# Performance work log

Hardware: AMD Instinct MI355X
Metric: run time of the kernel (lower is better)

Reference implementation:

```python
import jax, jax.numpy as jnp
import numpy as np

BN_EPS = 1e-5

def batchnorm(x, gamma, beta):
    # training-mode BatchNorm1d over the row (node/sample) dimension
    mu = jnp.mean(x, axis=0)
    var = jnp.var(x, axis=0)
    return (x - mu) * jax.lax.rsqrt(var + BN_EPS) * gamma + beta

def gin_mean(h, src, dst, n):
    # DGL GINConv(apply_func=None, aggregator='mean', eps=0):
    # h_new = h + mean_{u in N(v)} h_u
    ones = jnp.ones((src.shape[0],), h.dtype)
    deg = jax.ops.segment_sum(ones, dst, num_segments=n)
    agg = jax.ops.segment_sum(h[src], dst, num_segments=n)
    return h + agg / jnp.maximum(deg, 1.0)[:, None]

def setup_inputs() -> dict:
    key = jax.random.key(0)
    ks = jax.random.split(key, 12)
    N, E, B, K = 10000, 160000, 64, 10
    DIN, D, DH = 20, 512, 256
    x = jax.random.normal(ks[0], (N, DIN), dtype=jnp.float32)
    edge_src = jax.random.randint(ks[1], (E,), 0, N, dtype=jnp.int32)
    edge_dst = jax.random.randint(ks[2], (E,), 0, N, dtype=jnp.int32)
    node2graph = jnp.sort(jax.random.randint(ks[3], (N,), 0, B, dtype=jnp.int32))
    pg_emb = jax.random.normal(ks[4], (B, D), dtype=jnp.float32)
    neigh_emb = jax.random.normal(ks[5], (B, K, D), dtype=jnp.float32)
    s = lambda i, shp: jax.random.normal(ks[i], shp, dtype=jnp.float32) * 0.02
    return dict(
        x=x, pg_emb=pg_emb, neigh_emb=neigh_emb,
        W_init=s(6, (DIN, D)), b_init=jnp.zeros((D,), jnp.float32),
        g1=jnp.ones((D,), jnp.float32), be1=jnp.zeros((D,), jnp.float32),
        g2=jnp.ones((D,), jnp.float32), be2=jnp.zeros((D,), jnp.float32),
        W_fc=s(7, (3 * D, DH)), b_fc=jnp.zeros((DH,), jnp.float32),
        W_fc2=s(8, (DH, DH)), b_fc2=jnp.zeros((DH,), jnp.float32),
        W_fc3=s(9, (DH, DH)), b_fc3=jnp.zeros((DH,), jnp.float32),
        W_fc4=s(10, (DH, 1)), b_fc4=jnp.zeros((1,), jnp.float32),
        gb=jnp.ones((DH,), jnp.float32), bb=jnp.zeros((DH,), jnp.float32),
        gb2=jnp.ones((DH,), jnp.float32), bb2=jnp.zeros((DH,), jnp.float32),
        gb3=jnp.ones((DH,), jnp.float32), bb3=jnp.zeros((DH,), jnp.float32),
        edge_src=edge_src, edge_dst=edge_dst, node2graph=node2graph,
    )

def reference(x, pg_emb, neigh_emb, W_init, b_init, g1, be1, g2, be2,
              W_fc, b_fc, W_fc2, b_fc2, W_fc3, b_fc3, W_fc4, b_fc4,
              gb, bb, gb2, bb2, gb3, bb3, edge_src, edge_dst, node2graph):
    N = x.shape[0]
    B, K, D = neigh_emb.shape
    # two GIN(mean) layers with BN+ReLU on the batched graph
    h = x @ W_init + b_init                                   # [N, 512]
    h = jax.nn.relu(batchnorm(gin_mean(h, edge_src, edge_dst, N), g1, be1))
    h = jax.nn.relu(batchnorm(gin_mean(h, edge_src, edge_dst, N), g2, be2))
    # dgl.mean_nodes: per-graph mean readout
    cnt = jax.ops.segment_sum(jnp.ones((N,), h.dtype), node2graph, num_segments=B)
    qemb = jax.ops.segment_sum(h, node2graph, num_segments=B) / jnp.maximum(cnt, 1.0)[:, None]
    a = jnp.concatenate([qemb, pg_emb], axis=1)               # [B, 2D]
    a = jnp.broadcast_to(a[:, None, :], (B, K, 2 * D))        # repeat per candidate
    b = jnp.concatenate([a, neigh_emb], axis=-1).reshape(B * K, 3 * D)
    H = jax.nn.relu(batchnorm(b @ W_fc + b_fc, gb, bb))
    H2 = jax.nn.relu(batchnorm(H @ W_fc2 + b_fc2, gb2, bb2))
    H3 = jax.nn.relu(batchnorm(H2 @ W_fc3 + b_fc3, gb3, bb3))
    pred = jax.nn.sigmoid(H3 @ W_fc4 + b_fc4)                 # [B*K, 1]
    return pred.reshape(B, K)
```

## Files before the change

kernel.cpp:

```cpp
#include <hip/hip_runtime.h>
#include <hip/hip_bf16.h>
#include <math.h>

#define N_NODES 10000
#define N_EDGES 160000
#define D 512
#define DIN 20
#define B 64
#define KC 10
#define DH 256
#define NROW (B*KC)
#define BN_EPS 1e-5f

#define ZCOUNT 36352
#define Z4 (ZCOUNT/4)
#define D4 (N_NODES/4)
#define IM_ROWS 8
#define IM_UNITS (N_NODES/IM_ROWS)
#define GWAVES 4
#define GBLOCKS 1250
#define F1_NS 6
#define F1_ROWS 8
#define F1_KS 256

struct P {
  const float *x, *pg, *neigh, *Winit, *binit;
  const float *g1, *be1, *g2, *be2;
  const float *Wfc, *bfc, *W2, *b2, *W3, *b3, *W4, *b4;
  const float *gbA, *bbA, *gbB, *bbB, *gbC, *bbC;
  const int *esrc, *edst, *n2g;
  unsigned short *hb0, *hb1, *hb2;
  float *zbuf, *csum1, *csq1, *csum2, *csq2;
  float *s1,*q1,*s2,*q2,*s3,*q3, *qemb;
  float *G1,*G2,*G3,*part;
  int *degi,*rowstart,*cursor,*csr,*gstart;
  float *out;
};

__device__ __forceinline__ void f4acc(float4& a, const float4 v){
  a.x += v.x; a.y += v.y; a.z += v.z; a.w += v.w;
}
__device__ __forceinline__ void mk_affine(const float4 s, const float4 q, const float4 g,
                                          const float4 b, float4& sc, float4& sh){
  const float invN = 1.0f/(float)N_NODES;
  float mu, var, rs;
  mu = s.x*invN; var = q.x*invN - mu*mu; rs = rsqrtf(var+BN_EPS); sc.x = rs*g.x; sh.x = b.x - mu*sc.x;
  mu = s.y*invN; var = q.y*invN - mu*mu; rs = rsqrtf(var+BN_EPS); sc.y = rs*g.y; sh.y = b.y - mu*sc.y;
  mu = s.z*invN; var = q.z*invN - mu*mu; rs = rsqrtf(var+BN_EPS); sc.z = rs*g.z; sh.z = b.z - mu*sc.z;
  mu = s.w*invN; var = q.w*invN - mu*mu; rs = rsqrtf(var+BN_EPS); sc.w = rs*g.w; sh.w = b.w - mu*sc.w;
}
__device__ __forceinline__ float4 aff_relu(const float4 v, const float4 sc, const float4 sh){
  float4 o;
  o.x = fmaxf(fmaf(v.x, sc.x, sh.x), 0.0f);
  o.y = fmaxf(fmaf(v.y, sc.y, sh.y), 0.0f);
  o.z = fmaxf(fmaf(v.z, sc.z, sh.z), 0.0f);
  o.w = fmaxf(fmaf(v.w, sc.w, sh.w), 0.0f);
  return o;
}
__device__ __forceinline__ void bf_unpack(const uint4 u, float4& lo, float4& hi){
  lo.x = __uint_as_float(u.x << 16); lo.y = __uint_as_float(u.x & 0xffff0000u);
  lo.z = __uint_as_float(u.y << 16); lo.w = __uint_as_float(u.y & 0xffff0000u);
  hi.x = __uint_as_float(u.z << 16); hi.y = __uint_as_float(u.z & 0xffff0000u);
  hi.z = __uint_as_float(u.w << 16); hi.w = __uint_as_float(u.w & 0xffff0000u);
}
__device__ __forceinline__ unsigned bf_pack2(float a, float b){
  unsigned ua = __float_as_uint(a); ua = (ua + 0x7fffu + ((ua>>16)&1u)) >> 16;
  unsigned ub = __float_as_uint(b); ub = (ub + 0x7fffu + ((ub>>16)&1u)) & 0xffff0000u;
  return (ua & 0xffffu) | ub;
}
__device__ __forceinline__ unsigned short bf_pack1(float a){
  unsigned ua = __float_as_uint(a); return (unsigned short)((ua + 0x7fffu + ((ua>>16)&1u)) >> 16);
}

__global__ __launch_bounds__(256) void k_setup(P p){
  int b = blockIdx.x, nb = gridDim.x, t = threadIdx.x;
  for (int i4 = b*256 + t; i4 < Z4 + D4; i4 += nb*256){
    if (i4 < Z4) ((float4*)p.zbuf)[i4] = make_float4(0.f,0.f,0.f,0.f);
    else         ((int4*)p.degi)[i4 - Z4] = make_int4(0,0,0,0);
  }
  if (b == 0 && t <= B){
    int lo = 0, hi = N_NODES;
    while (lo < hi){ int mid = (lo+hi)>>1; if (p.n2g[mid] < t) lo = mid+1; else hi = mid; }
    p.gstart[t] = lo;
  }
}

__global__ __launch_bounds__(256) void k_deg(P p){
  int e = blockIdx.x*256 + threadIdx.x;
  if (e < N_EDGES) atomicAdd(&p.degi[p.edst[e]], 1);
}

__global__ __launch_bounds__(256) void k_scan(P p){
  __shared__ int part[256];
  int t = threadIdx.x;
  const int PER = (N_NODES + 255)/256;
  int base = t*PER;
  int s = 0;
  for (int i = 0; i < PER; ++i){ int idx = base+i; if (idx < N_NODES) s += p.degi[idx]; }
  part[t] = s;
  __syncthreads();
  for (int off = 1; off < 256; off <<= 1){
    int v = (t >= off) ? part[t-off] : 0;
    __syncthreads();
    part[t] += v;
    __syncthreads();
  }
  int run = (t > 0) ? part[t-1] : 0;
  for (int i = 0; i < PER; ++i){
    int idx = base+i;
    if (idx < N_NODES){ p.rowstart[idx] = run; p.cursor[idx] = run; run += p.degi[idx]; }
  }
  if (t == 255) p.rowstart[N_NODES] = run;
}

__global__ __launch_bounds__(256) void k_fill(P p){
  int e = blockIdx.x*256 + threadIdx.x;
  if (e < N_EDGES){
    int pos = atomicAdd(&p.cursor[p.edst[e]], 1);
    p.csr[pos] = p.esrc[e];
  }
}

__global__ __launch_bounds__(256) void k_init(P p){
  __shared__ float xs[IM_ROWS*DIN];
  int t = threadIdx.x;
  float wlo[DIN], whi[DIN];
  #pragma unroll
  for (int k = 0; k < DIN; ++k){ wlo[k] = p.Winit[k*D + t]; whi[k] = p.Winit[k*D + t + 256]; }
  float b0 = p.binit[t], b1 = p.binit[t+256];
  int r0 = blockIdx.x*IM_ROWS;
  for (int i = t; i < IM_ROWS*DIN; i += 256) xs[i] = p.x[(size_t)r0*DIN + i];
  __syncthreads();
  for (int rr = 0; rr < IM_ROWS; ++rr){
    float a0 = b0, a1 = b1;
    #pragma unroll
    for (int k = 0; k < DIN; ++k){
      float xv = xs[rr*DIN + k];
      a0 += xv*wlo[k]; a1 += xv*whi[k];
    }
    p.hb0[(size_t)(r0+rr)*D + t]       = bf_pack1(a0);
    p.hb0[(size_t)(r0+rr)*D + t + 256] = bf_pack1(a1);
  }
}

template<bool FUSED>
__device__ __forceinline__ void gather_body(const P& p,
    const unsigned short* __restrict__ hin, unsigned short* __restrict__ hout,
    const float* pcs, const float* pcq, const float* pgm, const float* pbt,
    float* cs, float* cq, float* red){
  int t = threadIdx.x;
  int lane = t & 63;
  int wave = t >> 6;
  int wid  = blockIdx.x*GWAVES + wave;
  int tot  = gridDim.x*GWAVES;
  const uint4* hb4 = (const uint4*)hin;
  float4 scA, shA, scB, shB;
  if (FUSED){
    mk_affine(((const float4*)pcs)[2*lane],   ((const float4*)pcq)[2*lane],
              ((const float4*)pgm)[2*lane],   ((const float4*)pbt)[2*lane],   scA, shA);
    mk_affine(((const float4*)pcs)[2*lane+1], ((const float4*)pcq)[2*lane+1],
              ((const float4*)pgm)[2*lane+1], ((const float4*)pbt)[2*lane+1], scB, shB);
  }
  float4 sLo = make_float4(0,0,0,0), sHi = make_float4(0,0,0,0);
  float4 qLo = make_float4(0,0,0,0), qHi = make_float4(0,0,0,0);
  for (int node = wid; node < N_NODES; node += tot){
    int start = p.rowstart[node], end = p.rowstart[node+1];
    float4 aLo = make_float4(0,0,0,0), aHi = make_float4(0,0,0,0);
    float4 bLo = make_float4(0,0,0,0), bHi = make_float4(0,0,0,0);
    for (int base = start; base < end; base += 64){
      int cnt = end - base; if (cnt > 64) cnt = 64;
      int myidx = (lane < cnt) ? p.csr[base+lane] : 0;
      int j = 0;
      for (; j+8 <= cnt; j += 8){
        uint4 u[8];
        #pragma unroll
        for (int k = 0; k < 8; ++k){
          int idx = __shfl(myidx, j+k, 64);
          u[k] = hb4[(size_t)idx*64 + lane];
        }
        #pragma unroll
        for (int k = 0; k < 8; ++k){
          float4 lo, hi; bf_unpack(u[k], lo, hi);
          if (FUSED){ lo = aff_relu(lo, scA, shA); hi = aff_relu(hi, scB, shB); }
          if (k & 1){ f4acc(bLo, lo); f4acc(bHi, hi); }
          else      { f4acc(aLo, lo); f4acc(aHi, hi); }
        }
      }
      for (; j < cnt; ++j){
        int idx = __shfl(myidx, j, 64);
        uint4 u0 = hb4[(size_t)idx*64 + lane];
        float4 lo, hi; bf_unpack(u0, lo, hi);
        if (FUSED){ lo = aff_relu(lo, scA, shA); hi = aff_relu(hi, scB, shB); }
        f4acc(aLo, lo); f4acc(aHi, hi);
      }
    }
    float inv = 1.0f/fmaxf((float)(end-start), 1.0f);
    uint4 us = hb4[(size_t)node*64 + lane];
    float4 hLo, hHi; bf_unpack(us, hLo, hHi);
    if (FUSED){ hLo = aff_relu(hLo, scA, shA); hHi = aff_relu(hHi, scB, shB); }
    float4 oLo, oHi;
    oLo.x = hLo.x + (aLo.x+bLo.x)*inv;  oLo.y = hLo.y + (aLo.y+bLo.y)*inv;
    oLo.z = hLo.z + (aLo.z+bLo.z)*inv;  oLo.w = hLo.w + (aLo.w+bLo.w)*inv;
    oHi.x = hHi.x + (aHi.x+bHi.x)*inv;  oHi.y = hHi.y + (aHi.y+bHi.y)*inv;
    oHi.z = hHi.z + (aHi.z+bHi.z)*inv;  oHi.w = hHi.w + (aHi.w+bHi.w)*inv;
    uint4 ou;
    ou.x = bf_pack2(oLo.x, oLo.y); ou.y = bf_pack2(oLo.z, oLo.w);
    ou.z = bf_pack2(oHi.x, oHi.y); ou.w = bf_pack2(oHi.z, oHi.w);
    ((uint4*)hout)[(size_t)node*64 + lane] = ou;
    f4acc(sLo, oLo); f4acc(sHi, oHi);
    qLo.x += oLo.x*oLo.x; qLo.y += oLo.y*oLo.y; qLo.z += oLo.z*oLo.z; qLo.w += oLo.w*oLo.w;
    qHi.x += oHi.x*oHi.x; qHi.y += oHi.y*oHi.y; qHi.z += oHi.z*oHi.z; qHi.w += oHi.w*oHi.w;
  }
  float* my = red + wave*1024;
  int c = 8*lane;
  *((float4*)&my[c])      = sLo;  *((float4*)&my[c+4])     = sHi;
  *((float4*)&my[512+c])  = qLo;  *((float4*)&my[512+c+4]) = qHi;
  __syncthreads();
  for (int e = t; e < 1024; e += 256){
    float v = red[e] + red[1024+e] + red[2048+e] + red[3072+e];
    if (e < 512) atomicAdd(&cs[e], v);
    else         atomicAdd(&cq[e-512], v);
  }
}

__global__ __launch_bounds__(256) void k_g1(P p){
  __shared__ float red[4096];
  gather_body<false>(p, p.hb0, p.hb1, nullptr,nullptr,nullptr,nullptr, p.csum1, p.csq1, red);
}
__global__ __launch_bounds__(256) void k_g2(P p){
  __shared__ float red[4096];
  gather_body<true>(p, p.hb1, p.hb2, p.csum1, p.csq1, p.g1, p.be1, p.csum2, p.csq2, red);
}

__global__ __launch_bounds__(256) void k_readout(P p){
  __shared__ float red[2048];
  int g = blockIdx.x >> 3, chunk = blockIdx.x & 7;
  int t = threadIdx.x;
  int lane = t & 63, wave = t >> 6;
  const uint4* hb4 = (const uint4*)p.hb2;
  float4 scA, shA, scB, shB;
  mk_affine(((const float4*)p.csum2)[2*lane],   ((const float4*)p.csq2)[2*lane],
            ((const float4*)p.g2)[2*lane],      ((const float4*)p.be2)[2*lane],   scA, shA);
  mk_affine(((const float4*)p.csum2)[2*lane+1], ((const float4*)p.csq2)[2*lane+1],
            ((const float4*)p.g2)[2*lane+1],    ((const float4*)p.be2)[2*lane+1], scB, shB);
  int s = p.gstart[g], e = p.gstart[g+1];
  int rows = e - s;
  int per = (rows + 7)/8;
  int r0 = s + chunk*per;
  int r1 = r0 + per; if (r1 > e) r1 = e;
  float4 aLo = make_float4(0,0,0,0), aHi = make_float4(0,0,0,0);
  for (int r = r0 + wave; r < r1; r += 4){
    uint4 u = hb4[(size_t)r*64 + lane];
    float4 lo, hi; bf_unpack(u, lo, hi);
    lo = aff_relu(lo, scA, shA); hi = aff_relu(hi, scB, shB);
    f4acc(aLo, lo); f4acc(aHi, hi);
  }
  int c = 8*lane;
  *((float4*)&red[wave*512 + c])     = aLo;
  *((float4*)&red[wave*512 + c + 4]) = aHi;
  __syncthreads();
  for (int e2 = t; e2 < 512; e2 += 256){
    float v = red[e2] + red[512+e2] + red[1024+e2] + red[1536+e2];
    atomicAdd(&p.qemb[(size_t)g*D + e2], v);
  }
}

__global__ __launch_bounds__(256) void k_fc1(P p){
  __shared__ float brow[F1_ROWS*F1_KS];
  int t = threadIdx.x;
  int rb = blockIdx.x % 80, ks = blockIdx.x / 80;
  int r0 = rb*F1_ROWS, k0 = ks*F1_KS;
  for (int rr = 0; rr < F1_ROWS; ++rr){
    int r = r0+rr;
    int g = r/KC, k = r - g*KC;
    int j = k0 + t;
    float v;
    if (j < D){
      float invc = 1.0f/fmaxf((float)(p.gstart[g+1]-p.gstart[g]), 1.0f);
      v = p.qemb[(size_t)g*D + j]*invc;
    } else if (j < 2*D){
      v = p.pg[(size_t)g*D + (j-D)];
    } else {
      v = p.neigh[((size_t)g*KC + k)*D + (j-2*D)];
    }
    brow[rr*F1_KS + t] = v;
  }
  __syncthreads();
  float acc[F1_ROWS] = {0.f,0.f,0.f,0.f,0.f,0.f,0.f,0.f};
  #pragma unroll 4
  for (int kk = 0; kk < F1_KS; ++kk){
    float w = p.Wfc[(size_t)(k0+kk)*DH + t];
    #pragma unroll
    for (int rr = 0; rr < F1_ROWS; ++rr) acc[rr] += brow[rr*F1_KS + kk]*w;
  }
  for (int rr = 0; rr < F1_ROWS; ++rr)
    p.part[((size_t)ks*NROW + r0+rr)*DH + t] = acc[rr];
}

__global__ __launch_bounds__(256) void k_reduce(P p){
  int t = threadIdx.x;
  int r0 = blockIdx.x*8;
  float bval = p.bfc[t];
  float ls = 0.f, lq = 0.f;
  for (int rr = 0; rr < 8; ++rr){
    int r = r0+rr;
    float acc = bval;
    for (int sl = 0; sl < F1_NS; ++sl) acc += p.part[((size_t)sl*NROW + r)*DH + t];
    p.G1[(size_t)r*DH + t] = acc;
    ls += acc; lq += acc*acc;
  }
  atomicAdd(&p.s1[t], ls); atomicAdd(&p.q1[t], lq);
}

__device__ __forceinline__ void fcmid_body(const float* in, const float* ps, const float* pq,
    const float* gamma, const float* beta, const float* W, const float* bias,
    float* outG, float* s, float* q, float* row){
  int t = threadIdx.x;
  int r = blockIdx.x;
  const float invM = 1.0f/(float)NROW;
  {
    float mu = ps[t]*invM;
    float var = pq[t]*invM - mu*mu;
    float rs = rsqrtf(var + BN_EPS);
    float v = in[(size_t)r*DH + t];
    row[t] = fmaxf((v-mu)*rs*gamma[t] + beta[t], 0.0f);
  }
  __syncthreads();
  float acc = bias[t];
  #pragma unroll 8
  for (int kk = 0; kk < DH; ++kk)
    acc += row[kk]*W[(size_t)kk*DH + t];
  outG[(size_t)r*DH + t] = acc;
  atomicAdd(&s[t], acc); atomicAdd(&q[t], acc*acc);
}
__global__ __launch_bounds__(256) void k_fc2(P p){ __shared__ float row[DH];
  fcmid_body(p.G1, p.s1, p.q1, p.gbA, p.bbA, p.W2, p.b2, p.G2, p.s2, p.q2, row); }
__global__ __launch_bounds__(256) void k_fc3(P p){ __shared__ float row[DH];
  fcmid_body(p.G2, p.s2, p.q2, p.gbB, p.bbB, p.W3, p.b3, p.G3, p.s3, p.q3, row); }

__global__ __launch_bounds__(256) void k_final(P p){
  int t = threadIdx.x;
  int wave = t>>6, lane = t&63;
  int r = blockIdx.x*4 + wave;
  const float invM = 1.0f/(float)NROW;
  float sum = 0.f;
  #pragma unroll
  for (int j = 0; j < 4; ++j){
    int c = lane + 64*j;
    float mu = p.s3[c]*invM;
    float var = p.q3[c]*invM - mu*mu;
    float rs = rsqrtf(var+BN_EPS);
    float v = p.G3[(size_t)r*DH + c];
    v = fmaxf((v-mu)*rs*p.gbC[c] + p.bbC[c], 0.0f);
    sum += v*p.W4[c];
  }
  #pragma unroll
  for (int off = 32; off > 0; off >>= 1) sum += __shfl_down(sum, off, 64);
  if (lane == 0){
    float z = sum + p.b4[0];
    p.out[r] = 1.0f/(1.0f + expf(-z));
  }
}

extern "C" void kernel_launch(void* const* d_in, const int* in_sizes, int n_in,
                              void* d_out, int out_size, void* d_ws, size_t ws_size,
                              hipStream_t stream) {
  P p;
  p.x     = (const float*)d_in[0];
  p.pg    = (const float*)d_in[1];
  p.neigh = (const float*)d_in[2];
  p.Winit = (const float*)d_in[3];
  p.binit = (const float*)d_in[4];
  p.g1    = (const float*)d_in[5];
  p.be1   = (const float*)d_in[6];
  p.g2    = (const float*)d_in[7];
  p.be2   = (const float*)d_in[8];
  p.Wfc   = (const float*)d_in[9];
  p.bfc   = (const float*)d_in[10];
  p.W2    = (const float*)d_in[11];
  p.b2    = (const float*)d_in[12];
  p.W3    = (const float*)d_in[13];
  p.b3    = (const float*)d_in[14];
  p.W4    = (const float*)d_in[15];
  p.b4    = (const float*)d_in[16];
  p.gbA   = (const float*)d_in[17];
  p.bbA   = (const float*)d_in[18];
  p.gbB   = (const float*)d_in[19];
  p.bbB   = (const float*)d_in[20];
  p.gbC   = (const float*)d_in[21];
  p.bbC   = (const float*)d_in[22];
  p.esrc  = (const int*)d_in[23];
  p.edst  = (const int*)d_in[24];
  p.n2g   = (const int*)d_in[25];
  p.out   = (float*)d_out;

  float* ws = (float*)d_ws;
  size_t off = 0;
  p.hb0 = (unsigned short*)(ws + off); off += (size_t)N_NODES*D/2;
  p.hb1 = (unsigned short*)(ws + off); off += (size_t)N_NODES*D/2;
  p.hb2 = (unsigned short*)(ws + off); off += (size_t)N_NODES*D/2;
  p.zbuf  = ws + off;
  p.csum1 = ws + off; off += 512;
  p.csq1  = ws + off; off += 512;
  p.csum2 = ws + off; off += 512;
  p.csq2  = ws + off; off += 512;
  p.s1    = ws + off; off += 256;
  p.q1    = ws + off; off += 256;
  p.s2    = ws + off; off += 256;
  p.q2    = ws + off; off += 256;
  p.s3    = ws + off; off += 256;
  p.q3    = ws + off; off += 256;
  p.qemb  = ws + off; off += (size_t)B*D;
  p.G1   = ws + off; off += (size_t)NROW*DH;
  p.G2   = ws + off; off += (size_t)NROW*DH;
  p.G3   = ws + off; off += (size_t)NROW*DH;
  p.part = ws + off; off += (size_t)F1_NS*NROW*DH;
  p.degi     = (int*)(ws + off); off += N_NODES;
  p.rowstart = (int*)(ws + off); off += N_NODES + 1;
  p.cursor   = (int*)(ws + off); off += N_NODES;
  p.csr      = (int*)(ws + off); off += N_EDGES;
  p.gstart   = (int*)(ws + off); off += B + 1;

  k_setup<<<64, 256, 0, stream>>>(p);
  k_deg<<<(N_EDGES+255)/256, 256, 0, stream>>>(p);
  k_scan<<<1, 256, 0, stream>>>(p);
  k_init<<<IM_UNITS, 256, 0, stream>>>(p);
  k_fill<<<(N_EDGES+255)/256, 256, 0, stream>>>(p);
  k_g1<<<GBLOCKS, 256, 0, stream>>>(p);
  k_g2<<<GBLOCKS, 256, 0, stream>>>(p);
  k_readout<<<512, 256, 0, stream>>>(p);
  k_fc1<<<480, 256, 0, stream>>>(p);
  k_reduce<<<80, 256, 0, stream>>>(p);
  k_fc2<<<NROW, 256, 0, stream>>>(p);
  k_fc3<<<NROW, 256, 0, stream>>>(p);
  k_final<<<NROW/4, 256, 0, stream>>>(p);
}
```

Before: 255.3 us.

## Software-pipeline neighbor gathers over two nodes per wave and fuse degree with init

The gather kernel now gives each wave exactly two nodes and interleaves their neighbor loads using double-buffered batches of eight rows. Predicated weights replace the tail loops, which raises memory-level parallelism in the latency-bound gather. The degree-count kernel is also merged into the initial projection kernel as extra blocks, removing one launch. The gather hardcodes 2 nodes per wave times 5000 waves, so it depends on GBLOCKS exactly covering N_NODES, and the deeper buffering raises register pressure.

```diff
diff --git a/kernel.cpp b/kernel.cpp
--- a/kernel.cpp
+++ b/kernel.cpp
@@ -17,6 +17,7 @@
 #define D4 (N_NODES/4)
 #define IM_ROWS 8
 #define IM_UNITS (N_NODES/IM_ROWS)
+#define DEG_BLOCKS 625
 #define GWAVES 4
 #define GBLOCKS 1250
 #define F1_NS 6
@@ -72,6 +73,140 @@
   unsigned ua = __float_as_uint(a); return (unsigned short)((ua + 0x7fffu + ((ua>>16)&1u)) >> 16);
 }
 
+struct Batch { uint4 v[8]; };
+
+__device__ __forceinline__ void load8(Batch& b, const uint4* __restrict__ hb4,
+                                      int idxreg, int k, int c, int lane){
+  #pragma unroll
+  for (int j = 0; j < 8; ++j){
+    int r = k*8 + j;
+    int ri = (r < c) ? r : (c-1);
+    int idx = __builtin_amdgcn_readlane(idxreg, ri);
+    b.v[j] = hb4[(size_t)idx*64 + lane];
+  }
+}
+
+template<bool FUSED>
+__device__ __forceinline__ void cons8(const Batch& b, int k, int c,
+    float4& accLo, float4& accHi,
+    const float4& scA, const float4& shA, const float4& scB, const float4& shB){
+  #pragma unroll
+  for (int j = 0; j < 8; ++j){
+    int r = k*8 + j;
+    float w = (r < c) ? 1.0f : 0.0f;
+    float4 lo, hi; bf_unpack(b.v[j], lo, hi);
+    if (FUSED){ lo = aff_relu(lo, scA, shA); hi = aff_relu(hi, scB, shB); }
+    accLo.x = fmaf(lo.x, w, accLo.x); accLo.y = fmaf(lo.y, w, accLo.y);
+    accLo.z = fmaf(lo.z, w, accLo.z); accLo.w = fmaf(lo.w, w, accLo.w);
+    accHi.x = fmaf(hi.x, w, accHi.x); accHi.y = fmaf(hi.y, w, accHi.y);
+    accHi.z = fmaf(hi.z, w, accHi.z); accHi.w = fmaf(hi.w, w, accHi.w);
+  }
+}
+
+template<bool FUSED>
+__device__ __forceinline__ void gather_body(const P& p,
+    const unsigned short* __restrict__ hin, unsigned short* __restrict__ hout,
+    const float* pcs, const float* pcq, const float* pgm, const float* pbt,
+    float* cs, float* cq, float* red){
+  int t = threadIdx.x;
+  int lane = t & 63;
+  int wave = t >> 6;
+  int wid  = blockIdx.x*GWAVES + wave;
+  int nA = 2*wid, nB = nA + 1;
+  const uint4* hb4 = (const uint4*)hin;
+  uint4 uSA = hb4[(size_t)nA*64 + lane];
+  uint4 uSB = hb4[(size_t)nB*64 + lane];
+  float4 scA, shA, scB, shB;
+  if (FUSED){
+    mk_affine(((const float4*)pcs)[2*lane],   ((const float4*)pcq)[2*lane],
+              ((const float4*)pgm)[2*lane],   ((const float4*)pbt)[2*lane],   scA, shA);
+    mk_affine(((const float4*)pcs)[2*lane+1], ((const float4*)pcq)[2*lane+1],
+              ((const float4*)pgm)[2*lane+1], ((const float4*)pbt)[2*lane+1], scB, shB);
+  }
+  int sA = p.rowstart[nA], sB = p.rowstart[nB], eB = p.rowstart[nB+1];
+  int cA = sB - sA, cB = eB - sB;
+  int idxA = (lane < cA) ? p.csr[sA + lane] : 0;
+  int idxB = (lane < cB) ? p.csr[sB + lane] : 0;
+  int cAf = (cA > 64) ? 64 : cA;
+  int cBf = (cB > 64) ? 64 : cB;
+  int bA = (cAf + 7) >> 3, bB = (cBf + 7) >> 3;
+  Batch A0, A1, B0, B1;
+  if (bA > 0) load8(A0, hb4, idxA, 0, cAf, lane);
+  if (bB > 0) load8(B0, hb4, idxB, 0, cBf, lane);
+  if (bA > 1) load8(A1, hb4, idxA, 1, cAf, lane);
+  if (bB > 1) load8(B1, hb4, idxB, 1, cBf, lane);
+  float4 aLoA = make_float4(0,0,0,0), aHiA = make_float4(0,0,0,0);
+  float4 aLoB = make_float4(0,0,0,0), aHiB = make_float4(0,0,0,0);
+  int ta = 0, tb = 0;
+  while (ta < bA || tb < bB){
+    if (ta < bA){ cons8<FUSED>(A0, ta, cAf, aLoA, aHiA, scA, shA, scB, shB);
+                  if (ta+2 < bA) load8(A0, hb4, idxA, ta+2, cAf, lane); ta++; }
+    if (tb < bB){ cons8<FUSED>(B0, tb, cBf, aLoB, aHiB, scA, shA, scB, shB);
+                  if (tb+2 < bB) load8(B0, hb4, idxB, tb+2, cBf, lane); tb++; }
+    if (ta < bA){ cons8<FUSED>(A1, ta, cAf, aLoA, aHiA, scA, shA, scB, shB);
+                  if (ta+2 < bA) load8(A1, hb4, idxA, ta+2, cAf, lane); ta++; }
+    if (tb < bB){ cons8<FUSED>(B1, tb, cBf, aLoB, aHiB, scA, shA, scB, shB);
+                  if (tb+2 < bB) load8(B1, hb4, idxB, tb+2, cBf, lane); tb++; }
+  }
+  for (int base = 64; base < cA; base += 64){
+    int cnt = cA - base; if (cnt > 64) cnt = 64;
+    int mi = (lane < cnt) ? p.csr[sA + base + lane] : 0;
+    for (int j = 0; j < cnt; ++j){
+      int idx = __builtin_amdgcn_readlane(mi, j);
+      uint4 u = hb4[(size_t)idx*64 + lane];
+      float4 lo, hi; bf_unpack(u, lo, hi);
+      if (FUSED){ lo = aff_relu(lo, scA, shA); hi = aff_relu(hi, scB, shB); }
+      f4acc(aLoA, lo); f4acc(aHiA, hi);
+    }
+  }
+  for (int base = 64; base < cB; base += 64){
+    int cnt = cB - base; if (cnt > 64) cnt = 64;
+    int mi = (lane < cnt) ? p.csr[sB + base + lane] : 0;
+    for (int j = 0; j < cnt; ++j){
+      int idx = __builtin_amdgcn_readlane(mi, j);
+      uint4 u = hb4[(size_t)idx*64 + lane];
+      float4 lo, hi; bf_unpack(u, lo, hi);
+      if (FUSED){ lo = aff_relu(lo, scA, shA); hi = aff_relu(hi, scB, shB); }
+      f4acc(aLoB, lo); f4acc(aHiB, hi);
+    }
+  }
+  float4 sLo = make_float4(0,0,0,0), sHi = make_float4(0,0,0,0);
+  float4 qLo = make_float4(0,0,0,0), qHi = make_float4(0,0,0,0);
+  #pragma unroll
+  for (int n = 0; n < 2; ++n){
+    int node = (n == 0) ? nA : nB;
+    int cnt  = (n == 0) ? cA : cB;
+    uint4 us = (n == 0) ? uSA : uSB;
+    float4 sumLo = (n == 0) ? aLoA : aLoB;
+    float4 sumHi = (n == 0) ? aHiA : aHiB;
+    float inv = 1.0f/fmaxf((float)cnt, 1.0f);
+    float4 hLo, hHi; bf_unpack(us, hLo, hHi);
+    if (FUSED){ hLo = aff_relu(hLo, scA, shA); hHi = aff_relu(hHi, scB, shB); }
+    float4 oLo, oHi;
+    oLo.x = hLo.x + sumLo.x*inv;  oLo.y = hLo.y + sumLo.y*inv;
+    oLo.z = hLo.z + sumLo.z*inv;  oLo.w = hLo.w + sumLo.w*inv;
+    oHi.x = hHi.x + sumHi.x*inv;  oHi.y = hHi.y + sumHi.y*inv;
+    oHi.z = hHi.z + sumHi.z*inv;  oHi.w = hHi.w + sumHi.w*inv;
+    uint4 ou;
+    ou.x = bf_pack2(oLo.x, oLo.y); ou.y = bf_pack2(oLo.z, oLo.w);
+    ou.z = bf_pack2(oHi.x, oHi.y); ou.w = bf_pack2(oHi.z, oHi.w);
+    ((uint4*)hout)[(size_t)node*64 + lane] = ou;
+    f4acc(sLo, oLo); f4acc(sHi, oHi);
+    qLo.x += oLo.x*oLo.x; qLo.y += oLo.y*oLo.y; qLo.z += oLo.z*oLo.z; qLo.w += oLo.w*oLo.w;
+    qHi.x += oHi.x*oHi.x; qHi.y += oHi.y*oHi.y; qHi.z += oHi.z*oHi.z; qHi.w += oHi.w*oHi.w;
+  }
+  float* my = red + wave*1024;
+  int c = 8*lane;
+  *((float4*)&my[c])      = sLo;  *((float4*)&my[c+4])     = sHi;
+  *((float4*)&my[512+c])  = qLo;  *((float4*)&my[512+c+4]) = qHi;
+  __syncthreads();
+  for (int e = t; e < 1024; e += 256){
+    float v = red[e] + red[1024+e] + red[2048+e] + red[3072+e];
+    if (e < 512) atomicAdd(&cs[e], v);
+    else         atomicAdd(&cq[e-512], v);
+  }
+}
+
 __global__ __launch_bounds__(256) void k_setup(P p){
   int b = blockIdx.x, nb = gridDim.x, t = threadIdx.x;
   for (int i4 = b*256 + t; i4 < Z4 + D4; i4 += nb*256){
@@ -85,50 +220,20 @@
   }
 }
 
-__global__ __launch_bounds__(256) void k_deg(P p){
-  int e = blockIdx.x*256 + threadIdx.x;
-  if (e < N_EDGES) atomicAdd(&p.degi[p.edst[e]], 1);
-}
-
-__global__ __launch_bounds__(256) void k_scan(P p){
-  __shared__ int part[256];
-  int t = threadIdx.x;
-  const int PER = (N_NODES + 255)/256;
-  int base = t*PER;
-  int s = 0;
-  for (int i = 0; i < PER; ++i){ int idx = base+i; if (idx < N_NODES) s += p.degi[idx]; }
-  part[t] = s;
-  __syncthreads();
-  for (int off = 1; off < 256; off <<= 1){
-    int v = (t >= off) ? part[t-off] : 0;
-    __syncthreads();
-    part[t] += v;
-    __syncthreads();
-  }
-  int run = (t > 0) ? part[t-1] : 0;
-  for (int i = 0; i < PER; ++i){
-    int idx = base+i;
-    if (idx < N_NODES){ p.rowstart[idx] = run; p.cursor[idx] = run; run += p.degi[idx]; }
-  }
-  if (t == 255) p.rowstart[N_NODES] = run;
-}
-
-__global__ __launch_bounds__(256) void k_fill(P p){
-  int e = blockIdx.x*256 + threadIdx.x;
-  if (e < N_EDGES){
-    int pos = atomicAdd(&p.cursor[p.edst[e]], 1);
-    p.csr[pos] = p.esrc[e];
-  }
-}
-
-__global__ __launch_bounds__(256) void k_init(P p){
+__global__ __launch_bounds__(256) void k_deg_init(P p){
   __shared__ float xs[IM_ROWS*DIN];
   int t = threadIdx.x;
+  if (blockIdx.x < DEG_BLOCKS){
+    int e = blockIdx.x*256 + t;
+    if (e < N_EDGES) atomicAdd(&p.degi[p.edst[e]], 1);
+    return;
+  }
+  int unit = blockIdx.x - DEG_BLOCKS;
   float wlo[DIN], whi[DIN];
   #pragma unroll
   for (int k = 0; k < DIN; ++k){ wlo[k] = p.Winit[k*D + t]; whi[k] = p.Winit[k*D + t + 256]; }
   float b0 = p.binit[t], b1 = p.binit[t+256];
-  int r0 = blockIdx.x*IM_ROWS;
+  int r0 = unit*IM_ROWS;
   for (int i = t; i < IM_ROWS*DIN; i += 256) xs[i] = p.x[(size_t)r0*DIN + i];
   __syncthreads();
   for (int rr = 0; rr < IM_ROWS; ++rr){
@@ -143,83 +248,34 @@
   }
 }
 
-template<bool FUSED>
-__device__ __forceinline__ void gather_body(const P& p,
-    const unsigned short* __restrict__ hin, unsigned short* __restrict__ hout,
-    const float* pcs, const float* pcq, const float* pgm, const float* pbt,
-    float* cs, float* cq, float* red){
-  int t = threadIdx.x;
-  int lane = t & 63;
-  int wave = t >> 6;
-  int wid  = blockIdx.x*GWAVES + wave;
-  int tot  = gridDim.x*GWAVES;
-  const uint4* hb4 = (const uint4*)hin;
-  float4 scA, shA, scB, shB;
-  if (FUSED){
-    mk_affine(((const float4*)pcs)[2*lane],   ((const float4*)pcq)[2*lane],
-              ((const float4*)pgm)[2*lane],   ((const float4*)pbt)[2*lane],   scA, shA);
-    mk_affine(((const float4*)pcs)[2*lane+1], ((const float4*)pcq)[2*lane+1],
-              ((const float4*)pgm)[2*lane+1], ((const float4*)pbt)[2*lane+1], scB, shB);
-  }
-  float4 sLo = make_float4(0,0,0,0), sHi = make_float4(0,0,0,0);
-  float4 qLo = make_float4(0,0,0,0), qHi = make_float4(0,0,0,0);
-  for (int node = wid; node < N_NODES; node += tot){
-    int start = p.rowstart[node], end = p.rowstart[node+1];
-    float4 aLo = make_float4(0,0,0,0), aHi = make_float4(0,0,0,0);
-    float4 bLo = make_float4(0,0,0,0), bHi = make_float4(0,0,0,0);
-    for (int base = start; base < end; base += 64){
-      int cnt = end - base; if (cnt > 64) cnt = 64;
-      int myidx = (lane < cnt) ? p.csr[base+lane] : 0;
-      int j = 0;
-      for (; j+8 <= cnt; j += 8){
-        uint4 u[8];
-        #pragma unroll
-        for (int k = 0; k < 8; ++k){
-          int idx = __shfl(myidx, j+k, 64);
-          u[k] = hb4[(size_t)idx*64 + lane];
-        }
-        #pragma unroll
-        for (int k = 0; k < 8; ++k){
-          float4 lo, hi; bf_unpack(u[k], lo, hi);
-          if (FUSED){ lo = aff_relu(lo, scA, shA); hi = aff_relu(hi, scB, shB); }
-          if (k & 1){ f4acc(bLo, lo); f4acc(bHi, hi); }
-          else      { f4acc(aLo, lo); f4acc(aHi, hi); }
-        }
-      }
-      for (; j < cnt; ++j){
-        int idx = __shfl(myidx, j, 64);
-        uint4 u0 = hb4[(size_t)idx*64 + lane];
-        float4 lo, hi; bf_unpack(u0, lo, hi);
-        if (FUSED){ lo = aff_relu(lo, scA, shA); hi = aff_relu(hi, scB, shB); }
-        f4acc(aLo, lo); f4acc(aHi, hi);
-      }
-    }
-    float inv = 1.0f/fmaxf((float)(end-start), 1.0f);
-    uint4 us = hb4[(size_t)node*64 + lane];
-    float4 hLo, hHi; bf_unpack(us, hLo, hHi);
-    if (FUSED){ hLo = aff_relu(hLo, scA, shA); hHi = aff_relu(hHi, scB, shB); }
-    float4 oLo, oHi;
-    oLo.x = hLo.x + (aLo.x+bLo.x)*inv;  oLo.y = hLo.y + (aLo.y+bLo.y)*inv;
-    oLo.z = hLo.z + (aLo.z+bLo.z)*inv;  oLo.w = hLo.w + (aLo.w+bLo.w)*inv;
-    oHi.x = hHi.x + (aHi.x+bHi.x)*inv;  oHi.y = hHi.y + (aHi.y+bHi.y)*inv;
-    oHi.z = hHi.z + (aHi.z+bHi.z)*inv;  oHi.w = hHi.w + (aHi.w+bHi.w)*inv;
-    uint4 ou;
-    ou.x = bf_pack2(oLo.x, oLo.y); ou.y = bf_pack2(oLo.z, oLo.w);
-    ou.z = bf_pack2(oHi.x, oHi.y); ou.w = bf_pack2(oHi.z, oHi.w);
-    ((uint4*)hout)[(size_t)node*64 + lane] = ou;
-    f4acc(sLo, oLo); f4acc(sHi, oHi);
-    qLo.x += oLo.x*oLo.x; qLo.y += oLo.y*oLo.y; qLo.z += oLo.z*oLo.z; qLo.w += oLo.w*oLo.w;
-    qHi.x += oHi.x*oHi.x; qHi.y += oHi.y*oHi.y; qHi.z += oHi.z*oHi.z; qHi.w += oHi.w*oHi.w;
-  }
-  float* my = red + wave*1024;
-  int c = 8*lane;
-  *((float4*)&my[c])      = sLo;  *((float4*)&my[c+4])     = sHi;
-  *((float4*)&my[512+c])  = qLo;  *((float4*)&my[512+c+4]) = qHi;
-  __syncthreads();
-  for (int e = t; e < 1024; e += 256){
-    float v = red[e] + red[1024+e] + red[2048+e] + red[3072+e];
-    if (e < 512) atomicAdd(&cs[e], v);
-    else         atomicAdd(&cq[e-512], v);
+__global__ __launch_bounds__(256) void k_scan(P p){
+  __shared__ int part[256];
+  int t = threadIdx.x;
+  const int PER = (N_NODES + 255)/256;
+  int base = t*PER;
+  int s = 0;
+  for (int i = 0; i < PER; ++i){ int idx = base+i; if (idx < N_NODES) s += p.degi[idx]; }
+  part[t] = s;
+  __syncthreads();
+  for (int off = 1; off < 256; off <<= 1){
+    int v = (t >= off) ? part[t-off] : 0;
+    __syncthreads();
+    part[t] += v;
+    __syncthreads();
+  }
+  int run = (t > 0) ? part[t-1] : 0;
+  for (int i = 0; i < PER; ++i){
+    int idx = base+i;
+    if (idx < N_NODES){ p.rowstart[idx] = run; p.cursor[idx] = run; run += p.degi[idx]; }
+  }
+  if (t == 255) p.rowstart[N_NODES] = run;
+}
+
+__global__ __launch_bounds__(256) void k_fill(P p){
+  int e = blockIdx.x*256 + threadIdx.x;
+  if (e < N_EDGES){
+    int pos = atomicAdd(&p.cursor[p.edst[e]], 1);
+    p.csr[pos] = p.esrc[e];
   }
 }
 
@@ -422,9 +478,8 @@
   p.gstart   = (int*)(ws + off); off += B + 1;
 
   k_setup<<<64, 256, 0, stream>>>(p);
-  k_deg<<<(N_EDGES+255)/256, 256, 0, stream>>>(p);
+  k_deg_init<<<DEG_BLOCKS + IM_UNITS, 256, 0, stream>>>(p);
   k_scan<<<1, 256, 0, stream>>>(p);
-  k_init<<<IM_UNITS, 256, 0, stream>>>(p);
   k_fill<<<(N_EDGES+255)/256, 256, 0, stream>>>(p);
   k_g1<<<GBLOCKS, 256, 0, stream>>>(p);
   k_g2<<<GBLOCKS, 256, 0, stream>>>(p);
```

After: 252.9 us. No clear change (-0.9%).

## Merge degree count with init matmul and split-K tile FC2/FC3 with row reuse

Applied to the files above, without the earlier changes.

The degree-count and input-projection kernels become one launch, with block ranges assigned to each task. This removes a launch and lets the two run at the same time. FC2 and FC3 now compute 4 rows per block over a 2-way K split, so each loaded weight is reused across rows. The partial results go to a buffer and a shared reduce kernel adds the bias and accumulates the BN statistics. This cuts weight traffic and per-row atomics but adds two extra reduce launches.

```diff
diff --git a/kernel.cpp b/kernel.cpp
--- a/kernel.cpp
+++ b/kernel.cpp
@@ -17,11 +17,15 @@
 #define D4 (N_NODES/4)
 #define IM_ROWS 8
 #define IM_UNITS (N_NODES/IM_ROWS)
+#define DEG_BLOCKS 625
 #define GWAVES 4
 #define GBLOCKS 1250
 #define F1_NS 6
 #define F1_ROWS 8
 #define F1_KS 256
+#define FM_ROWS 4
+#define FM_KS 128
+#define FM_NS 2
 
 struct P {
   const float *x, *pg, *neigh, *Winit, *binit;
@@ -70,77 +74,6 @@
 }
 __device__ __forceinline__ unsigned short bf_pack1(float a){
   unsigned ua = __float_as_uint(a); return (unsigned short)((ua + 0x7fffu + ((ua>>16)&1u)) >> 16);
-}
-
-__global__ __launch_bounds__(256) void k_setup(P p){
-  int b = blockIdx.x, nb = gridDim.x, t = threadIdx.x;
-  for (int i4 = b*256 + t; i4 < Z4 + D4; i4 += nb*256){
-    if (i4 < Z4) ((float4*)p.zbuf)[i4] = make_float4(0.f,0.f,0.f,0.f);
-    else         ((int4*)p.degi)[i4 - Z4] = make_int4(0,0,0,0);
-  }
-  if (b == 0 && t <= B){
-    int lo = 0, hi = N_NODES;
-    while (lo < hi){ int mid = (lo+hi)>>1; if (p.n2g[mid] < t) lo = mid+1; else hi = mid; }
-    p.gstart[t] = lo;
-  }
-}
-
-__global__ __launch_bounds__(256) void k_deg(P p){
-  int e = blockIdx.x*256 + threadIdx.x;
-  if (e < N_EDGES) atomicAdd(&p.degi[p.edst[e]], 1);
-}
-
-__global__ __launch_bounds__(256) void k_scan(P p){
-  __shared__ int part[256];
-  int t = threadIdx.x;
-  const int PER = (N_NODES + 255)/256;
-  int base = t*PER;
-  int s = 0;
-  for (int i = 0; i < PER; ++i){ int idx = base+i; if (idx < N_NODES) s += p.degi[idx]; }
-  part[t] = s;
-  __syncthreads();
-  for (int off = 1; off < 256; off <<= 1){
-    int v = (t >= off) ? part[t-off] : 0;
-    __syncthreads();
-    part[t] += v;
-    __syncthreads();
-  }
-  int run = (t > 0) ? part[t-1] : 0;
-  for (int i = 0; i < PER; ++i){
-    int idx = base+i;
-    if (idx < N_NODES){ p.rowstart[idx] = run; p.cursor[idx] = run; run += p.degi[idx]; }
-  }
-  if (t == 255) p.rowstart[N_NODES] = run;
-}
-
-__global__ __launch_bounds__(256) void k_fill(P p){
-  int e = blockIdx.x*256 + threadIdx.x;
-  if (e < N_EDGES){
-    int pos = atomicAdd(&p.cursor[p.edst[e]], 1);
-    p.csr[pos] = p.esrc[e];
-  }
-}
-
-__global__ __launch_bounds__(256) void k_init(P p){
-  __shared__ float xs[IM_ROWS*DIN];
-  int t = threadIdx.x;
-  float wlo[DIN], whi[DIN];
-  #pragma unroll
-  for (int k = 0; k < DIN; ++k){ wlo[k] = p.Winit[k*D + t]; whi[k] = p.Winit[k*D + t + 256]; }
-  float b0 = p.binit[t], b1 = p.binit[t+256];
-  int r0 = blockIdx.x*IM_ROWS;
-  for (int i = t; i < IM_ROWS*DIN; i += 256) xs[i] = p.x[(size_t)r0*DIN + i];
-  __syncthreads();
-  for (int rr = 0; rr < IM_ROWS; ++rr){
-    float a0 = b0, a1 = b1;
-    #pragma unroll
-    for (int k = 0; k < DIN; ++k){
-      float xv = xs[rr*DIN + k];
-      a0 += xv*wlo[k]; a1 += xv*whi[k];
-    }
-    p.hb0[(size_t)(r0+rr)*D + t]       = bf_pack1(a0);
-    p.hb0[(size_t)(r0+rr)*D + t + 256] = bf_pack1(a1);
-  }
 }
 
 template<bool FUSED>
@@ -223,6 +156,78 @@
   }
 }
 
+__global__ __launch_bounds__(256) void k_setup(P p){
+  int b = blockIdx.x, nb = gridDim.x, t = threadIdx.x;
+  for (int i4 = b*256 + t; i4 < Z4 + D4; i4 += nb*256){
+    if (i4 < Z4) ((float4*)p.zbuf)[i4] = make_float4(0.f,0.f,0.f,0.f);
+    else         ((int4*)p.degi)[i4 - Z4] = make_int4(0,0,0,0);
+  }
+  if (b == 0 && t <= B){
+    int lo = 0, hi = N_NODES;
+    while (lo < hi){ int mid = (lo+hi)>>1; if (p.n2g[mid] < t) lo = mid+1; else hi = mid; }
+    p.gstart[t] = lo;
+  }
+}
+
+__global__ __launch_bounds__(256) void k_deg_init(P p){
+  __shared__ float xs[IM_ROWS*DIN];
+  int t = threadIdx.x;
+  if (blockIdx.x < DEG_BLOCKS){
+    int e = blockIdx.x*256 + t;
+    if (e < N_EDGES) atomicAdd(&p.degi[p.edst[e]], 1);
+    return;
+  }
+  int unit = blockIdx.x - DEG_BLOCKS;
+  float wlo[DIN], whi[DIN];
+  #pragma unroll
+  for (int k = 0; k < DIN; ++k){ wlo[k] = p.Winit[k*D + t]; whi[k] = p.Winit[k*D + t + 256]; }
+  float b0 = p.binit[t], b1 = p.binit[t+256];
+  int r0 = unit*IM_ROWS;
+  for (int i = t; i < IM_ROWS*DIN; i += 256) xs[i] = p.x[(size_t)r0*DIN + i];
+  __syncthreads();
+  for (int rr = 0; rr < IM_ROWS; ++rr){
+    float a0 = b0, a1 = b1;
+    #pragma unroll
+    for (int k = 0; k < DIN; ++k){
+      float xv = xs[rr*DIN + k];
+      a0 += xv*wlo[k]; a1 += xv*whi[k];
+    }
+    p.hb0[(size_t)(r0+rr)*D + t]       = bf_pack1(a0);
+    p.hb0[(size_t)(r0+rr)*D + t + 256] = bf_pack1(a1);
+  }
+}
+
+__global__ __launch_bounds__(256) void k_scan(P p){
+  __shared__ int part[256];
+  int t = threadIdx.x;
+  const int PER = (N_NODES + 255)/256;
+  int base = t*PER;
+  int s = 0;
+  for (int i = 0; i < PER; ++i){ int idx = base+i; if (idx < N_NODES) s += p.degi[idx]; }
+  part[t] = s;
+  __syncthreads();
+  for (int off = 1; off < 256; off <<= 1){
+    int v = (t >= off) ? part[t-off] : 0;
+    __syncthreads();
+    part[t] += v;
+    __syncthreads();
+  }
+  int run = (t > 0) ? part[t-1] : 0;
+  for (int i = 0; i < PER; ++i){
+    int idx = base+i;
+    if (idx < N_NODES){ p.rowstart[idx] = run; p.cursor[idx] = run; run += p.degi[idx]; }
+  }
+  if (t == 255) p.rowstart[N_NODES] = run;
+}
+
+__global__ __launch_bounds__(256) void k_fill(P p){
+  int e = blockIdx.x*256 + threadIdx.x;
+  if (e < N_EDGES){
+    int pos = atomicAdd(&p.cursor[p.edst[e]], 1);
+    p.csr[pos] = p.esrc[e];
+  }
+}
+
 __global__ __launch_bounds__(256) void k_g1(P p){
   __shared__ float red[4096];
   gather_body<false>(p, p.hb0, p.hb1, nullptr,nullptr,nullptr,nullptr, p.csum1, p.csq1, red);
@@ -297,46 +302,51 @@
     p.part[((size_t)ks*NROW + r0+rr)*DH + t] = acc[rr];
 }
 
-__global__ __launch_bounds__(256) void k_reduce(P p){
+__global__ __launch_bounds__(256) void k_reduce(P p, const float* bias, float* outG,
+                                                float* s, float* q, int nslice){
   int t = threadIdx.x;
   int r0 = blockIdx.x*8;
-  float bval = p.bfc[t];
+  float bval = bias[t];
   float ls = 0.f, lq = 0.f;
   for (int rr = 0; rr < 8; ++rr){
     int r = r0+rr;
     float acc = bval;
-    for (int sl = 0; sl < F1_NS; ++sl) acc += p.part[((size_t)sl*NROW + r)*DH + t];
-    p.G1[(size_t)r*DH + t] = acc;
+    for (int sl = 0; sl < nslice; ++sl) acc += p.part[((size_t)sl*NROW + r)*DH + t];
+    outG[(size_t)r*DH + t] = acc;
     ls += acc; lq += acc*acc;
   }
-  atomicAdd(&p.s1[t], ls); atomicAdd(&p.q1[t], lq);
-}
-
-__device__ __forceinline__ void fcmid_body(const float* in, const float* ps, const float* pq,
-    const float* gamma, const float* beta, const float* W, const float* bias,
-    float* outG, float* s, float* q, float* row){
-  int t = threadIdx.x;
-  int r = blockIdx.x;
+  atomicAdd(&s[t], ls); atomicAdd(&q[t], lq);
+}
+
+__global__ __launch_bounds__(256) void k_fcmid(P p, const float* in, const float* ps,
+    const float* pq, const float* gamma, const float* beta, const float* W){
+  __shared__ float row[FM_ROWS*FM_KS];
+  int t = threadIdx.x;
+  int r0 = blockIdx.x*FM_ROWS;
+  int k0 = blockIdx.y*FM_KS;
   const float invM = 1.0f/(float)NROW;
-  {
-    float mu = ps[t]*invM;
-    float var = pq[t]*invM - mu*mu;
+  #pragma unroll
+  for (int i = 0; i < 2; ++i){
+    int idx = t + i*256;
+    int rr = idx >> 7, kk = idx & 127;
+    int c = k0 + kk;
+    float mu = ps[c]*invM;
+    float var = pq[c]*invM - mu*mu;
     float rs = rsqrtf(var + BN_EPS);
-    float v = in[(size_t)r*DH + t];
-    row[t] = fmaxf((v-mu)*rs*gamma[t] + beta[t], 0.0f);
-  }
-  __syncthreads();
-  float acc = bias[t];
-  #pragma unroll 8
-  for (int kk = 0; kk < DH; ++kk)
-    acc += row[kk]*W[(size_t)kk*DH + t];
-  outG[(size_t)r*DH + t] = acc;
-  atomicAdd(&s[t], acc); atomicAdd(&q[t], acc*acc);
-}
-__global__ __launch_bounds__(256) void k_fc2(P p){ __shared__ float row[DH];
-  fcmid_body(p.G1, p.s1, p.q1, p.gbA, p.bbA, p.W2, p.b2, p.G2, p.s2, p.q2, row); }
-__global__ __launch_bounds__(256) void k_fc3(P p){ __shared__ float row[DH];
-  fcmid_body(p.G2, p.s2, p.q2, p.gbB, p.bbB, p.W3, p.b3, p.G3, p.s3, p.q3, row); }
+    float v = in[(size_t)(r0+rr)*DH + c];
+    row[rr*FM_KS + kk] = fmaxf((v-mu)*rs*gamma[c] + beta[c], 0.0f);
+  }
+  __syncthreads();
+  float acc[FM_ROWS] = {0.f,0.f,0.f,0.f};
+  #pragma unroll 4
+  for (int kk = 0; kk < FM_KS; ++kk){
+    float w = W[(size_t)(k0+kk)*DH + t];
+    #pragma unroll
+    for (int rr = 0; rr < FM_ROWS; ++rr) acc[rr] += row[rr*FM_KS + kk]*w;
+  }
+  for (int rr = 0; rr < FM_ROWS; ++rr)
+    p.part[((size_t)blockIdx.y*NROW + r0+rr)*DH + t] = acc[rr];
+}
 
 __global__ __launch_bounds__(256) void k_final(P p){
   int t = threadIdx.x;
@@ -422,16 +432,17 @@
   p.gstart   = (int*)(ws + off); off += B + 1;
 
   k_setup<<<64, 256, 0, stream>>>(p);
-  k_deg<<<(N_EDGES+255)/256, 256, 0, stream>>>(p);
+  k_deg_init<<<DEG_BLOCKS + IM_UNITS, 256, 0, stream>>>(p);
   k_scan<<<1, 256, 0, stream>>>(p);
-  k_init<<<IM_UNITS, 256, 0, stream>>>(p);
   k_fill<<<(N_EDGES+255)/256, 256, 0, stream>>>(p);
   k_g1<<<GBLOCKS, 256, 0, stream>>>(p);
   k_g2<<<GBLOCKS, 256, 0, stream>>>(p);
   k_readout<<<512, 256, 0, stream>>>(p);
   k_fc1<<<480, 256, 0, stream>>>(p);
-  k_reduce<<<80, 256, 0, stream>>>(p);
-  k_fc2<<<NROW, 256, 0, stream>>>(p);
-  k_fc3<<<NROW, 256, 0, stream>>>(p);
+  k_reduce<<<NROW/8, 256, 0, stream>>>(p, p.bfc, p.G1, p.s1, p.q1, F1_NS);
+  k_fcmid<<<dim3(NROW/FM_ROWS, FM_NS), 256, 0, stream>>>(p, p.G1, p.s1, p.q1, p.gbA, p.bbA, p.W2);
+  k_reduce<<<NROW/8, 256, 0, stream>>>(p, p.b2, p.G2, p.s2, p.q2, FM_NS);
+  k_fcmid<<<dim3(NROW/FM_ROWS, FM_NS), 256, 0, stream>>>(p, p.G2, p.s2, p.q2, p.gbB, p.bbB, p.W3);
+  k_reduce<<<NROW/8, 256, 0, stream>>>(p, p.b3, p.G3, p.s3, p.q3, FM_NS);
   k_final<<<NROW/4, 256, 0, stream>>>(p);
 }
```

After: 240.5 us. -5.8%, faster.
